# Kernel optimization log

Hardware: AMD Instinct MI355X
Metric: run time of the kernel (lower is better)

The kernel has to match this reference:

```python
import jax, jax.numpy as jnp
import numpy as np

B, S, H = 2, 2048, 2048
FFN = 1024
E = 8
TOP_K = 2


def setup_inputs() -> dict:
    key = jax.random.key(0)
    ks = jax.random.split(key, 5)
    scale = 0.02
    hidden_states = jax.random.normal(ks[0], (B, S, H), dtype=jnp.float32)
    Wg = jax.random.normal(ks[1], (E, H), dtype=jnp.float32) * scale   # gate: Linear(H, E) weight
    W1 = jax.random.normal(ks[2], (E, FFN, H), dtype=jnp.float32) * scale  # stacked w1 per expert
    W3 = jax.random.normal(ks[3], (E, FFN, H), dtype=jnp.float32) * scale  # stacked w3 per expert
    W2 = jax.random.normal(ks[4], (E, H, FFN), dtype=jnp.float32) * scale  # stacked w2 per expert
    bias = jnp.zeros((E,), dtype=jnp.float32)  # e_score_correction_bias buffer
    return {"hidden_states": hidden_states, "Wg": Wg, "W1": W1, "W2": W2, "W3": W3, "bias": bias}


def reference(hidden_states, Wg, W1, W2, W3, bias):
    bsz, seq_len, hidden_dim = hidden_states.shape
    x = hidden_states.reshape(-1, hidden_dim)                 # [T, H]
    router_logits = x @ Wg.T                                  # [T, E]
    routing_weights = jax.nn.sigmoid(router_logits.astype(jnp.float32))
    scores = routing_weights + bias                           # bias only affects selection
    _, top_k_index = jax.lax.top_k(scores, TOP_K)             # [T, K]
    top_k_weights = jnp.take_along_axis(routing_weights, top_k_index, axis=1)
    top_k_weights = top_k_weights / top_k_weights.sum(axis=-1, keepdims=True)
    top_k_weights = top_k_weights.astype(x.dtype)
    # per-token per-expert combine weight (0 for non-selected experts)
    one_hot = jax.nn.one_hot(top_k_index, Wg.shape[0], dtype=x.dtype)  # [T, K, E]
    expert_w = jnp.einsum('tk,tke->te', top_k_weights, one_hot)        # [T, E]
    # SwiGLU expert MLPs applied via stacked (grouped) GEMMs
    h1 = jnp.einsum('th,efh->tef', x, W1)                     # [T, E, FFN]
    h3 = jnp.einsum('th,efh->tef', x, W3)
    g = jax.nn.silu(h1) * h3 * expert_w[:, :, None]           # scale before down-proj
    out = jnp.einsum('tef,ehf->th', g, W2)                    # weighted combine
    return out.reshape(bsz, seq_len, hidden_dim)
```

## Files before the change

### kernel.cpp

```cpp
#include <hip/hip_runtime.h>
#include <hip/hip_bf16.h>


#define T_TOK 4096
#define H_DIM 2048
#define FFN_D 1024
#define NE    8

typedef __attribute__((ext_vector_type(8))) short          bf16x8;
typedef __attribute__((ext_vector_type(4))) float          f32x4;
typedef __attribute__((ext_vector_type(4))) unsigned short us4;

#define N4_PER_W ((size_t)NE * FFN_D * H_DIM / 4)
#define RB_ROUTER 1024u
#define CB_CONV   8192u

__device__ __forceinline__ unsigned short f2bf(float f) {
  unsigned u = __builtin_bit_cast(unsigned, f);
  u += 0x7fffu + ((u >> 16) & 1u);
  return (unsigned short)(u >> 16);
}
__device__ __forceinline__ float bf2f(unsigned short u) {
  return __builtin_bit_cast(float, ((unsigned)u) << 16);
}
__device__ __forceinline__ us4 f4bf(float4 v) {
  union { us4 o; unsigned u[2]; } r;
  asm("v_cvt_pk_bf16_f32 %0, %1, %2" : "=v"(r.u[0]) : "v"(v.x), "v"(v.y));
  asm("v_cvt_pk_bf16_f32 %0, %1, %2" : "=v"(r.u[1]) : "v"(v.z), "v"(v.w));
  return r.o;
}
__device__ __forceinline__ void async16(const void* g, void* l) {
  __builtin_amdgcn_global_load_lds((const __attribute__((address_space(1))) void*)g,
                                   (__attribute__((address_space(3))) void*)l, 16, 0, 0);
}

__global__ void router_conv_kernel(const float* __restrict__ x,
                                   const float* __restrict__ Wg,
                                   const float* __restrict__ bias,
                                   unsigned* __restrict__ epair,
                                   float* __restrict__ wpair,
                                   unsigned short* __restrict__ Xb,
                                   const float* __restrict__ W1, unsigned short* __restrict__ W1b,
                                   const float* __restrict__ W3, unsigned short* __restrict__ W3b) {
  if (blockIdx.x >= RB_ROUTER) {
    size_t b0 = (size_t)(blockIdx.x - RB_ROUTER) * 1024;
#pragma unroll
    for (int k = 0; k < 4; k++) {
      size_t i = b0 + k * 256 + threadIdx.x;
      const float* s; unsigned short* d;
      if (i < N4_PER_W) { s = W1; d = W1b; } else { s = W3; d = W3b; i -= N4_PER_W; }
      float4 v = ((const float4*)s)[i];
      ((us4*)d)[i] = f4bf(v);
    }
    return;
  }
  const int wv   = threadIdx.x >> 6;
  const int lane = threadIdx.x & 63;
  const int t    = blockIdx.x * 4 + wv;

  const float4* xr = (const float4*)(x + (size_t)t * H_DIM);
  us4*          xb = (us4*)(Xb + (size_t)t * H_DIM);

  float acc[NE];
#pragma unroll
  for (int e = 0; e < NE; e++) acc[e] = 0.f;

#pragma unroll
  for (int j = 0; j < 8; j++) {
    int i4 = j * 64 + lane;
    float4 v = xr[i4];
    xb[i4] = f4bf(v);
#pragma unroll
    for (int e = 0; e < NE; e++) {
      float4 w = ((const float4*)(Wg + e * H_DIM))[i4];
      acc[e] += v.x * w.x + v.y * w.y + v.z * w.z + v.w * w.w;
    }
  }
#pragma unroll
  for (int e = 0; e < NE; e++) {
#pragma unroll
    for (int m = 32; m >= 1; m >>= 1) acc[e] += __shfl_xor(acc[e], m, 64);
  }

  if (lane == 0) {
    float sig[NE], sc[NE];
#pragma unroll
    for (int e = 0; e < NE; e++) {
      sig[e] = 1.f / (1.f + expf(-acc[e]));
      sc[e]  = sig[e] + bias[e];
    }
    int i1 = 0; float v1 = sc[0];
#pragma unroll
    for (int e = 1; e < NE; e++) if (sc[e] > v1) { v1 = sc[e]; i1 = e; }
    int i2 = -1; float v2 = -1e30f;
#pragma unroll
    for (int e = 0; e < NE; e++) if (e != i1 && sc[e] > v2) { v2 = sc[e]; i2 = e; }
    float w1 = sig[i1], w2 = sig[i2];
    float s = w1 + w2;
    epair[t] = (unsigned)i1 | ((unsigned)i2 << 8);
    wpair[2 * t]     = w1 / s;
    wpair[2 * t + 1] = w2 / s;
  }
}

__global__ void compact_kernel(const unsigned* __restrict__ epair,
                               const float* __restrict__ wpair,
                               int* __restrict__ cnt,
                               int* __restrict__ base,
                               int* __restrict__ rows,
                               float* __restrict__ wts,
                               int* __restrict__ t2s) {
  const int e    = threadIdx.x >> 6;
  const int lane = threadIdx.x & 63;
  const unsigned long long ltmask = ((unsigned long long)1 << lane) - 1;
  __shared__ int cnts[NE];

  int count = 0;
  for (int c = 0; c < T_TOK; c += 64) {
    int t = c + lane;
    unsigned ep = epair[t];
    bool m1 = ((ep & 255u) == (unsigned)e);
    bool m2 = (((ep >> 8) & 255u) == (unsigned)e);
    unsigned long long b1 = __ballot(m1);
    if (m1) {
      int p = count + __popcll(b1 & ltmask);
      rows[e * T_TOK + p] = t;
      wts [e * T_TOK + p] = wpair[2 * t];
      t2s[2 * t] = (e << 12) | p;
    }
    count += __popcll(b1);
    unsigned long long b2 = __ballot(m2);
    if (m2) {
      int p = count + __popcll(b2 & ltmask);
      rows[e * T_TOK + p] = t;
      wts [e * T_TOK + p] = wpair[2 * t + 1];
      t2s[2 * t + 1] = (e << 12) | p;
    }
    count += __popcll(b2);
  }
  if (lane == 0) { cnts[e] = count; cnt[e] = count; }
  __syncthreads();
  if (threadIdx.x == 0) {
    int s = 0;
    for (int i = 0; i < NE; i++) { base[i] = s; s += cnts[i]; }
    base[NE] = s;
  }
}

__launch_bounds__(256)
__global__ void upproj_fast(const unsigned short* __restrict__ Xb,
                            const unsigned short* __restrict__ W1b,
                            const unsigned short* __restrict__ W3b,
                            const int* __restrict__ cnt,
                            const int* __restrict__ base,
                            const int* __restrict__ rows,
                            const float* __restrict__ wts,
                            unsigned short* __restrict__ G,
                            const float* __restrict__ W2, unsigned short* __restrict__ W2b) {
  if (blockIdx.z == NE) {
    size_t flat = (size_t)blockIdx.y * 16 + blockIdx.x;
    size_t b0 = flat * 8192;
#pragma unroll
    for (int k = 0; k < 32; k++) {
      size_t i = b0 + (size_t)k * 256 + threadIdx.x;
      float4 v = ((const float4*)W2)[i];
      ((us4*)W2b)[i] = f4bf(v);
    }
    return;
  }
  const int e  = blockIdx.z;
  const int m0 = blockIdx.y * 128;
  const int n0 = blockIdx.x * 64;
  const int ce = cnt[e];
  if (m0 >= ce) return;

  __shared__ __align__(16) unsigned short As [3][128 * 32];
  __shared__ __align__(16) unsigned short B1s[3][64 * 32];
  __shared__ __align__(16) unsigned short B3s[3][64 * 32];
  __shared__ int   t_ids[128];
  __shared__ float w_lds[128];

  const int tid = threadIdx.x;
  if (tid < 128) {
    int i = m0 + tid;
    if (i < ce) { t_ids[tid] = rows[e * T_TOK + i]; w_lds[tid] = wts[e * T_TOK + i]; }
    else        { t_ids[tid] = 0;                   w_lds[tid] = 0.f; }
  }
  __syncthreads();

  const int lane = tid & 63;
  const int wv   = tid >> 6;

  const int sA   = (lane >> 3) & 3;
  const int gcol = ((lane & 3) ^ sA) * 8;
  const int rxor = ((lane & 15) >> 1) & 3;
  const int qx   = ((lane >> 4) ^ rxor) * 8;

  const unsigned short* gA[2];
#pragma unroll
  for (int c = 0; c < 2; c++) {
    int r = wv * 32 + c * 16 + (lane >> 2);
    gA[c] = Xb + (size_t)t_ids[r] * H_DIM + gcol;
  }
  const size_t wrow = (size_t)(n0 + wv * 16 + (lane >> 2));
  const unsigned short* gB1 = W1b + (size_t)e * FFN_D * H_DIM + wrow * H_DIM + gcol;
  const unsigned short* gB3 = W3b + (size_t)e * FFN_D * H_DIM + wrow * H_DIM + gcol;
  const int dA0 = (wv * 32 + 0)  * 32;
  const int dA1 = (wv * 32 + 16) * 32;
  const int dB  = (wv * 16) * 32;

  const int wm = (wv & 1) * 64;
  const int wn = (wv >> 1) * 32;
  const int lr = lane & 15;

  f32x4 acc1[4][2], acc3[4][2];
#pragma unroll
  for (int mi = 0; mi < 4; mi++)
#pragma unroll
    for (int ni = 0; ni < 2; ni++) { acc1[mi][ni] = (f32x4)0.f; acc3[mi][ni] = (f32x4)0.f; }

#define STAGE_UP(KT, BUF)                          \
  do {                                             \
    async16(gA[0] + (KT), &As [BUF][dA0]);         \
    async16(gA[1] + (KT), &As [BUF][dA1]);         \
    async16(gB1  + (KT), &B1s[BUF][dB]);           \
    async16(gB3  + (KT), &B3s[BUF][dB]);           \
  } while (0)

  STAGE_UP(0, 0);
  STAGE_UP(32, 1);
  asm volatile("s_waitcnt vmcnt(4)" ::: "memory");
  __builtin_amdgcn_s_barrier();

  for (int k = 0; k < H_DIM / 32; ++k) {
    const int kt2 = (k + 2) * 32;
    const int cb  = k % 3;
    if (kt2 < H_DIM) STAGE_UP(kt2, (k + 2) % 3);
    __builtin_amdgcn_sched_barrier(0);

    bf16x8 a[4], b1[2], b3[2];
#pragma unroll
    for (int mi = 0; mi < 4; mi++)
      a[mi] = *(const bf16x8*)&As[cb][(wm + mi * 16 + lr) * 32 + qx];
#pragma unroll
    for (int ni = 0; ni < 2; ni++) {
      b1[ni] = *(const bf16x8*)&B1s[cb][(wn + ni * 16 + lr) * 32 + qx];
      b3[ni] = *(const bf16x8*)&B3s[cb][(wn + ni * 16 + lr) * 32 + qx];
    }
#pragma unroll
    for (int mi = 0; mi < 4; mi++)
#pragma unroll
      for (int ni = 0; ni < 2; ni++) {
        acc1[mi][ni] = __builtin_amdgcn_mfma_f32_16x16x32_bf16(a[mi], b1[ni], acc1[mi][ni], 0, 0, 0);
        acc3[mi][ni] = __builtin_amdgcn_mfma_f32_16x16x32_bf16(a[mi], b3[ni], acc3[mi][ni], 0, 0, 0);
      }

    if (kt2 < H_DIM) asm volatile("s_waitcnt vmcnt(4)" ::: "memory");
    else             asm volatile("s_waitcnt vmcnt(0)" ::: "memory");
    __builtin_amdgcn_sched_barrier(0);
    __builtin_amdgcn_s_barrier();
    __builtin_amdgcn_sched_barrier(0);
  }
#undef STAGE_UP

  const int be = base[e];
#pragma unroll
  for (int mi = 0; mi < 4; mi++)
#pragma unroll
    for (int ni = 0; ni < 2; ni++)
#pragma unroll
      for (int r = 0; r < 4; r++) {
        int row = wm + mi * 16 + (lane >> 4) * 4 + r;
        int col = wn + ni * 16 + lr;
        int i = m0 + row;
        if (i < ce) {
          float h1 = acc1[mi][ni][r];
          float h3 = acc3[mi][ni][r];
          float g  = h1 / (1.f + expf(-h1)) * h3 * w_lds[row];
          G[(size_t)(be + i) * FFN_D + n0 + col] = f2bf(g);
        }
      }
}

__launch_bounds__(256)
__global__ void downproj_fast(const unsigned short* __restrict__ G,
                              const unsigned short* __restrict__ W2b,
                              const int* __restrict__ cnt,
                              const int* __restrict__ base,
                              unsigned short* __restrict__ Gd) {
  const int e  = blockIdx.z;
  const int m0 = blockIdx.y * 128;
  const int n0 = blockIdx.x * 128;
  const int ce = cnt[e];
  if (m0 >= ce) return;
  const int be = base[e];

  __shared__ __align__(16) unsigned short As[3][128 * 32];
  __shared__ __align__(16) unsigned short Bs[3][128 * 32];

  const int tid  = threadIdx.x;
  const int lane = tid & 63;
  const int wv   = tid >> 6;

  const int sA   = (lane >> 3) & 3;
  const int gcol = ((lane & 3) ^ sA) * 8;
  const int rxor = ((lane & 15) >> 1) & 3;
  const int qx   = ((lane >> 4) ^ rxor) * 8;

  const unsigned short* gA[2];
  const unsigned short* gB[2];
#pragma unroll
  for (int c = 0; c < 2; c++) {
    int r = m0 + wv * 32 + c * 16 + (lane >> 2);
    if (r >= ce) r = ce - 1;
    gA[c] = G + (size_t)(be + r) * FFN_D + gcol;
    int rb = wv * 32 + c * 16 + (lane >> 2);
    gB[c] = W2b + (size_t)e * H_DIM * FFN_D + (size_t)(n0 + rb) * FFN_D + gcol;
  }
  const int dA0 = (wv * 32 + 0)  * 32;
  const int dA1 = (wv * 32 + 16) * 32;

  const int wm = (wv & 1) * 64;
  const int wn = (wv >> 1) * 64;
  const int lr = lane & 15;

  f32x4 acc[4][4];
#pragma unroll
  for (int mi = 0; mi < 4; mi++)
#pragma unroll
    for (int ni = 0; ni < 4; ni++) acc[mi][ni] = (f32x4)0.f;

#define STAGE_DN(KT, BUF)                          \
  do {                                             \
    async16(gA[0] + (KT), &As[BUF][dA0]);          \
    async16(gA[1] + (KT), &As[BUF][dA1]);          \
    async16(gB[0] + (KT), &Bs[BUF][dA0]);          \
    async16(gB[1] + (KT), &Bs[BUF][dA1]);          \
  } while (0)

  STAGE_DN(0, 0);
  STAGE_DN(32, 1);
  asm volatile("s_waitcnt vmcnt(4)" ::: "memory");
  __builtin_amdgcn_s_barrier();

  for (int k = 0; k < FFN_D / 32; ++k) {
    const int kt2 = (k + 2) * 32;
    const int cb  = k % 3;
    if (kt2 < FFN_D) STAGE_DN(kt2, (k + 2) % 3);
    __builtin_amdgcn_sched_barrier(0);

    bf16x8 a[4], b[4];
#pragma unroll
    for (int mi = 0; mi < 4; mi++)
      a[mi] = *(const bf16x8*)&As[cb][(wm + mi * 16 + lr) * 32 + qx];
#pragma unroll
    for (int ni = 0; ni < 4; ni++)
      b[ni] = *(const bf16x8*)&Bs[cb][(wn + ni * 16 + lr) * 32 + qx];
#pragma unroll
    for (int mi = 0; mi < 4; mi++)
#pragma unroll
      for (int ni = 0; ni < 4; ni++)
        acc[mi][ni] = __builtin_amdgcn_mfma_f32_16x16x32_bf16(a[mi], b[ni], acc[mi][ni], 0, 0, 0);

    if (kt2 < FFN_D) asm volatile("s_waitcnt vmcnt(4)" ::: "memory");
    else             asm volatile("s_waitcnt vmcnt(0)" ::: "memory");
    __builtin_amdgcn_sched_barrier(0);
    __builtin_amdgcn_s_barrier();
    __builtin_amdgcn_sched_barrier(0);
  }
#undef STAGE_DN

#pragma unroll
  for (int mi = 0; mi < 4; mi++)
#pragma unroll
    for (int ni = 0; ni < 4; ni++)
#pragma unroll
      for (int r = 0; r < 4; r++) {
        int row = wm + mi * 16 + (lane >> 4) * 4 + r;
        int col = wn + ni * 16 + lr;
        int i = m0 + row;
        if (i < ce)
          Gd[(size_t)(be + i) * H_DIM + n0 + col] = f2bf(acc[mi][ni][r]);
      }
}

__global__ void combine_kernel(const unsigned short* __restrict__ Gd,
                               const int* __restrict__ base,
                               const int* __restrict__ tok2slot,
                               float* __restrict__ out) {
  const int t = blockIdx.x;
  const int v1 = tok2slot[2 * t], v2 = tok2slot[2 * t + 1];
  const int s1 = base[v1 >> 12] + (v1 & 4095);
  const int s2 = base[v2 >> 12] + (v2 & 4095);
  const us4* r1 = (const us4*)(Gd + (size_t)s1 * H_DIM);
  const us4* r2 = (const us4*)(Gd + (size_t)s2 * H_DIM);
  float4* o = (float4*)(out + (size_t)t * H_DIM);
#pragma unroll
  for (int j = 0; j < 2; j++) {
    int i = j * 256 + threadIdx.x;
    us4 a = r1[i], b = r2[i];
    float4 r;
    r.x = bf2f(a.x) + bf2f(b.x);
    r.y = bf2f(a.y) + bf2f(b.y);
    r.z = bf2f(a.z) + bf2f(b.z);
    r.w = bf2f(a.w) + bf2f(b.w);
    o[i] = r;
  }
}

extern "C" void kernel_launch(void* const* d_in, const int* in_sizes, int n_in,
                              void* d_out, int out_size, void* d_ws, size_t ws_size,
                              hipStream_t stream) {
  (void)in_sizes; (void)n_in; (void)out_size; (void)ws_size;
  const float* x    = (const float*)d_in[0];
  const float* Wg   = (const float*)d_in[1];
  const float* W1   = (const float*)d_in[2];
  const float* W2   = (const float*)d_in[3];
  const float* W3   = (const float*)d_in[4];
  const float* bias = (const float*)d_in[5];
  float* out = (float*)d_out;

  char* ws = (char*)d_ws;
  const size_t OFF_CNT   = 0;
  const size_t OFF_BASE  = 64;
  const size_t OFF_T2S   = 1024;
  const size_t OFF_ROWS  = 65536;
  const size_t OFF_WTS   = OFF_ROWS + 131072;
  const size_t OFF_EPAIR = OFF_WTS + 131072;
  const size_t OFF_WPAIR = OFF_EPAIR + 16384;
  const size_t OFF_XB    = 1048576;
  const size_t OFF_W1B   = OFF_XB + 16777216;
  const size_t OFF_W3B   = OFF_W1B + 33554432;
  const size_t OFF_G     = OFF_W3B + 33554432;
  const size_t OFF_W2B   = OFF_G + 16777216;

  int*   cnt   = (int*)(ws + OFF_CNT);
  int*   base  = (int*)(ws + OFF_BASE);
  int*   t2s   = (int*)(ws + OFF_T2S);
  int*   rows  = (int*)(ws + OFF_ROWS);
  float* wts   = (float*)(ws + OFF_WTS);
  unsigned* epair = (unsigned*)(ws + OFF_EPAIR);
  float* wpair = (float*)(ws + OFF_WPAIR);
  unsigned short* Xb  = (unsigned short*)(ws + OFF_XB);
  unsigned short* W1b = (unsigned short*)(ws + OFF_W1B);
  unsigned short* W3b = (unsigned short*)(ws + OFF_W3B);
  unsigned short* W2b = (unsigned short*)(ws + OFF_W2B);
  unsigned short* Gd  = (unsigned short*)(ws + OFF_W1B);
  unsigned short* G   = (unsigned short*)(ws + OFF_G);

  router_conv_kernel<<<RB_ROUTER + CB_CONV, 256, 0, stream>>>(
      x, Wg, bias, epair, wpair, Xb, W1, W1b, W3, W3b);

  compact_kernel<<<1, 512, 0, stream>>>(epair, wpair, cnt, base, rows, wts, t2s);

  dim3 g2(FFN_D / 64, T_TOK / 128, NE + 1);
  upproj_fast<<<g2, 256, 0, stream>>>(Xb, W1b, W3b, cnt, base, rows, wts, G, W2, W2b);

  dim3 g3(H_DIM / 128, T_TOK / 128, NE);
  downproj_fast<<<g3, 256, 0, stream>>>(G, W2b, cnt, base, Gd);

  combine_kernel<<<T_TOK, 256, 0, stream>>>(Gd, base, t2s, out);
}
```

Baseline: 453.3 us.

## Restructure expert GEMMs into 8-wave, 64-deep two-phase pipelined tiles and move W2 conversion

```diff
diff --git a/kernel.cpp b/kernel.cpp
--- a/kernel.cpp
+++ b/kernel.cpp
@@ -14,6 +14,7 @@
 #define N4_PER_W ((size_t)NE * FFN_D * H_DIM / 4)
 #define RB_ROUTER 1024u
 #define CB_CONV   8192u
+#define CB_W2     4096u
 
 __device__ __forceinline__ unsigned short f2bf(float f) {
   unsigned u = __builtin_bit_cast(unsigned, f);
@@ -41,7 +42,18 @@
                                    float* __restrict__ wpair,
                                    unsigned short* __restrict__ Xb,
                                    const float* __restrict__ W1, unsigned short* __restrict__ W1b,
-                                   const float* __restrict__ W3, unsigned short* __restrict__ W3b) {
+                                   const float* __restrict__ W3, unsigned short* __restrict__ W3b,
+                                   const float* __restrict__ W2, unsigned short* __restrict__ W2b) {
+  if (blockIdx.x >= RB_ROUTER + CB_CONV) {
+    size_t b0 = (size_t)(blockIdx.x - RB_ROUTER - CB_CONV) * 1024;
+#pragma unroll
+    for (int k = 0; k < 4; k++) {
+      size_t i = b0 + k * 256 + threadIdx.x;
+      float4 v = ((const float4*)W2)[i];
+      ((us4*)W2b)[i] = f4bf(v);
+    }
+    return;
+  }
   if (blockIdx.x >= RB_ROUTER) {
     size_t b0 = (size_t)(blockIdx.x - RB_ROUTER) * 1024;
 #pragma unroll
@@ -147,71 +159,56 @@
   }
 }
 
-__launch_bounds__(256)
-__global__ void upproj_fast(const unsigned short* __restrict__ Xb,
-                            const unsigned short* __restrict__ W1b,
-                            const unsigned short* __restrict__ W3b,
-                            const int* __restrict__ cnt,
-                            const int* __restrict__ base,
-                            const int* __restrict__ rows,
-                            const float* __restrict__ wts,
-                            unsigned short* __restrict__ G,
-                            const float* __restrict__ W2, unsigned short* __restrict__ W2b) {
-  if (blockIdx.z == NE) {
-    size_t flat = (size_t)blockIdx.y * 16 + blockIdx.x;
-    size_t b0 = flat * 8192;
-#pragma unroll
-    for (int k = 0; k < 32; k++) {
-      size_t i = b0 + (size_t)k * 256 + threadIdx.x;
-      float4 v = ((const float4*)W2)[i];
-      ((us4*)W2b)[i] = f4bf(v);
-    }
-    return;
-  }
+__launch_bounds__(512)
+__global__ void upproj_8ph(const unsigned short* __restrict__ Xb,
+                           const unsigned short* __restrict__ W1b,
+                           const unsigned short* __restrict__ W3b,
+                           const int* __restrict__ cnt,
+                           const int* __restrict__ base,
+                           const int* __restrict__ rows,
+                           const float* __restrict__ wts,
+                           unsigned short* __restrict__ G) {
   const int e  = blockIdx.z;
-  const int m0 = blockIdx.y * 128;
+  const int m0 = blockIdx.y * 256;
   const int n0 = blockIdx.x * 64;
   const int ce = cnt[e];
   if (m0 >= ce) return;
 
-  __shared__ __align__(16) unsigned short As [3][128 * 32];
-  __shared__ __align__(16) unsigned short B1s[3][64 * 32];
-  __shared__ __align__(16) unsigned short B3s[3][64 * 32];
-  __shared__ int   t_ids[128];
-  __shared__ float w_lds[128];
+  __shared__ __align__(16) unsigned short As [3][256 * 64];
+  __shared__ __align__(16) unsigned short B1s[3][64 * 64];
+  __shared__ __align__(16) unsigned short B3s[3][64 * 64];
+  __shared__ int   t_ids[256];
+  __shared__ float w_lds[256];
 
   const int tid = threadIdx.x;
-  if (tid < 128) {
+  if (tid < 256) {
     int i = m0 + tid;
     if (i < ce) { t_ids[tid] = rows[e * T_TOK + i]; w_lds[tid] = wts[e * T_TOK + i]; }
     else        { t_ids[tid] = 0;                   w_lds[tid] = 0.f; }
   }
   __syncthreads();
 
-  const int lane = tid & 63;
-  const int wv   = tid >> 6;
-
-  const int sA   = (lane >> 3) & 3;
-  const int gcol = ((lane & 3) ^ sA) * 8;
-  const int rxor = ((lane & 15) >> 1) & 3;
-  const int qx   = ((lane >> 4) ^ rxor) * 8;
-
-  const unsigned short* gA[2];
-#pragma unroll
-  for (int c = 0; c < 2; c++) {
-    int r = wv * 32 + c * 16 + (lane >> 2);
-    gA[c] = Xb + (size_t)t_ids[r] * H_DIM + gcol;
-  }
-  const size_t wrow = (size_t)(n0 + wv * 16 + (lane >> 2));
-  const unsigned short* gB1 = W1b + (size_t)e * FFN_D * H_DIM + wrow * H_DIM + gcol;
-  const unsigned short* gB3 = W3b + (size_t)e * FFN_D * H_DIM + wrow * H_DIM + gcol;
-  const int dA0 = (wv * 32 + 0)  * 32;
-  const int dA1 = (wv * 32 + 16) * 32;
-  const int dB  = (wv * 16) * 32;
-
-  const int wm = (wv & 1) * 64;
-  const int wn = (wv >> 1) * 32;
-  const int lr = lane & 15;
+  const int lane  = tid & 63;
+  const int wv    = tid >> 6;
+  const int srow8 = lane >> 3;
+  const int scol  = ((lane & 7) ^ srow8) * 8;
+
+  const unsigned short* apA[4];
+#pragma unroll
+  for (int j = 0; j < 4; j++) {
+    int r = j * 64 + wv * 8 + srow8;
+    apA[j] = Xb + (size_t)t_ids[r] * H_DIM + scol;
+  }
+  const size_t ebase = (size_t)e * FFN_D * H_DIM;
+  const int rbw = wv * 8 + srow8;
+  const unsigned short* apB1 = W1b + ebase + (size_t)(n0 + rbw) * H_DIM + scol;
+  const unsigned short* apB3 = W3b + ebase + (size_t)(n0 + rbw) * H_DIM + scol;
+
+  const int wvM = wv >> 1;
+  const int wvN = wv & 1;
+  const int fr  = lane & 15;
+  const int hi  = lane >> 4;
+  const int rx  = fr & 7;
 
   f32x4 acc1[4][2], acc3[4][2];
 #pragma unroll
@@ -219,34 +216,43 @@
 #pragma unroll
     for (int ni = 0; ni < 2; ni++) { acc1[mi][ni] = (f32x4)0.f; acc3[mi][ni] = (f32x4)0.f; }
 
-#define STAGE_UP(KT, BUF)                          \
-  do {                                             \
-    async16(gA[0] + (KT), &As [BUF][dA0]);         \
-    async16(gA[1] + (KT), &As [BUF][dA1]);         \
-    async16(gB1  + (KT), &B1s[BUF][dB]);           \
-    async16(gB3  + (KT), &B3s[BUF][dB]);           \
-  } while (0)
-
-  STAGE_UP(0, 0);
-  STAGE_UP(32, 1);
-  asm volatile("s_waitcnt vmcnt(4)" ::: "memory");
+#define UPS_A3(T, B) { int kk = (T) * 64;                      \
+    async16(apA[0] + kk, &As[B][(  0 + wv * 8) * 64]);         \
+    async16(apA[1] + kk, &As[B][( 64 + wv * 8) * 64]);         \
+    async16(apA[2] + kk, &As[B][(128 + wv * 8) * 64]); }
+#define UPS_AB(T, B) { int kk = (T) * 64;                      \
+    async16(apA[3] + kk, &As[B][(192 + wv * 8) * 64]);         \
+    async16(apB1 + kk,  &B1s[B][(wv * 8) * 64]);               \
+    async16(apB3 + kk,  &B3s[B][(wv * 8) * 64]); }
+
+  UPS_A3(0, 0) UPS_AB(0, 0)
+  UPS_A3(1, 1) UPS_AB(1, 1)
+  asm volatile("s_waitcnt vmcnt(6)" ::: "memory");
   __builtin_amdgcn_s_barrier();
 
-  for (int k = 0; k < H_DIM / 32; ++k) {
-    const int kt2 = (k + 2) * 32;
-    const int cb  = k % 3;
-    if (kt2 < H_DIM) STAGE_UP(kt2, (k + 2) % 3);
-    __builtin_amdgcn_sched_barrier(0);
-
+  for (int t = 0; t < H_DIM / 64; ++t) {
+    const int  cb = t % 3;
+    const int  nb = (t + 2) % 3;
+    const bool pf = (t + 2 < H_DIM / 64);
+
+    if (pf) UPS_A3(t + 2, nb)
     bf16x8 a[4], b1[2], b3[2];
-#pragma unroll
-    for (int mi = 0; mi < 4; mi++)
-      a[mi] = *(const bf16x8*)&As[cb][(wm + mi * 16 + lr) * 32 + qx];
-#pragma unroll
-    for (int ni = 0; ni < 2; ni++) {
-      b1[ni] = *(const bf16x8*)&B1s[cb][(wn + ni * 16 + lr) * 32 + qx];
-      b3[ni] = *(const bf16x8*)&B3s[cb][(wn + ni * 16 + lr) * 32 + qx];
-    }
+    {
+      const int c = ((0 + hi) ^ rx) * 8;
+#pragma unroll
+      for (int mi = 0; mi < 4; mi++)
+        a[mi] = *(const bf16x8*)&As[cb][(wvM * 64 + mi * 16 + fr) * 64 + c];
+#pragma unroll
+      for (int ni = 0; ni < 2; ni++) {
+        b1[ni] = *(const bf16x8*)&B1s[cb][(wvN * 32 + ni * 16 + fr) * 64 + c];
+        b3[ni] = *(const bf16x8*)&B3s[cb][(wvN * 32 + ni * 16 + fr) * 64 + c];
+      }
+    }
+    __builtin_amdgcn_sched_barrier(0);
+    __builtin_amdgcn_s_barrier();
+    asm volatile("s_waitcnt lgkmcnt(0)" ::: "memory");
+    __builtin_amdgcn_sched_barrier(0);
+    __builtin_amdgcn_s_setprio(1);
 #pragma unroll
     for (int mi = 0; mi < 4; mi++)
 #pragma unroll
@@ -254,14 +260,42 @@
         acc1[mi][ni] = __builtin_amdgcn_mfma_f32_16x16x32_bf16(a[mi], b1[ni], acc1[mi][ni], 0, 0, 0);
         acc3[mi][ni] = __builtin_amdgcn_mfma_f32_16x16x32_bf16(a[mi], b3[ni], acc3[mi][ni], 0, 0, 0);
       }
-
-    if (kt2 < H_DIM) asm volatile("s_waitcnt vmcnt(4)" ::: "memory");
-    else             asm volatile("s_waitcnt vmcnt(0)" ::: "memory");
-    __builtin_amdgcn_sched_barrier(0);
-    __builtin_amdgcn_s_barrier();
-    __builtin_amdgcn_sched_barrier(0);
-  }
-#undef STAGE_UP
+    __builtin_amdgcn_s_setprio(0);
+    __builtin_amdgcn_sched_barrier(0);
+    __builtin_amdgcn_s_barrier();
+
+    if (pf) UPS_AB(t + 2, nb)
+    {
+      const int c = ((4 + hi) ^ rx) * 8;
+#pragma unroll
+      for (int mi = 0; mi < 4; mi++)
+        a[mi] = *(const bf16x8*)&As[cb][(wvM * 64 + mi * 16 + fr) * 64 + c];
+#pragma unroll
+      for (int ni = 0; ni < 2; ni++) {
+        b1[ni] = *(const bf16x8*)&B1s[cb][(wvN * 32 + ni * 16 + fr) * 64 + c];
+        b3[ni] = *(const bf16x8*)&B3s[cb][(wvN * 32 + ni * 16 + fr) * 64 + c];
+      }
+    }
+    __builtin_amdgcn_sched_barrier(0);
+    if (pf) asm volatile("s_waitcnt vmcnt(6)" ::: "memory");
+    else    asm volatile("s_waitcnt vmcnt(0)" ::: "memory");
+    __builtin_amdgcn_s_barrier();
+    asm volatile("s_waitcnt lgkmcnt(0)" ::: "memory");
+    __builtin_amdgcn_sched_barrier(0);
+    __builtin_amdgcn_s_setprio(1);
+#pragma unroll
+    for (int mi = 0; mi < 4; mi++)
+#pragma unroll
+      for (int ni = 0; ni < 2; ni++) {
+        acc1[mi][ni] = __builtin_amdgcn_mfma_f32_16x16x32_bf16(a[mi], b1[ni], acc1[mi][ni], 0, 0, 0);
+        acc3[mi][ni] = __builtin_amdgcn_mfma_f32_16x16x32_bf16(a[mi], b3[ni], acc3[mi][ni], 0, 0, 0);
+      }
+    __builtin_amdgcn_s_setprio(0);
+    __builtin_amdgcn_sched_barrier(0);
+    __builtin_amdgcn_s_barrier();
+  }
+#undef UPS_A3
+#undef UPS_AB
 
   const int be = base[e];
 #pragma unroll
@@ -270,8 +304,8 @@
     for (int ni = 0; ni < 2; ni++)
 #pragma unroll
       for (int r = 0; r < 4; r++) {
-        int row = wm + mi * 16 + (lane >> 4) * 4 + r;
-        int col = wn + ni * 16 + lr;
+        int row = wvM * 64 + mi * 16 + hi * 4 + r;
+        int col = wvN * 32 + ni * 16 + fr;
         int i = m0 + row;
         if (i < ce) {
           float h1 = acc1[mi][ni][r];
@@ -282,47 +316,46 @@
       }
 }
 
-__launch_bounds__(256)
-__global__ void downproj_fast(const unsigned short* __restrict__ G,
-                              const unsigned short* __restrict__ W2b,
-                              const int* __restrict__ cnt,
-                              const int* __restrict__ base,
-                              unsigned short* __restrict__ Gd) {
+__launch_bounds__(512)
+__global__ void downproj_8ph(const unsigned short* __restrict__ G,
+                             const unsigned short* __restrict__ W2b,
+                             const int* __restrict__ cnt,
+                             const int* __restrict__ base,
+                             unsigned short* __restrict__ Gd) {
   const int e  = blockIdx.z;
-  const int m0 = blockIdx.y * 128;
+  const int m0 = blockIdx.y * 256;
   const int n0 = blockIdx.x * 128;
   const int ce = cnt[e];
   if (m0 >= ce) return;
   const int be = base[e];
 
-  __shared__ __align__(16) unsigned short As[3][128 * 32];
-  __shared__ __align__(16) unsigned short Bs[3][128 * 32];
-
-  const int tid  = threadIdx.x;
-  const int lane = tid & 63;
-  const int wv   = tid >> 6;
-
-  const int sA   = (lane >> 3) & 3;
-  const int gcol = ((lane & 3) ^ sA) * 8;
-  const int rxor = ((lane & 15) >> 1) & 3;
-  const int qx   = ((lane >> 4) ^ rxor) * 8;
-
-  const unsigned short* gA[2];
-  const unsigned short* gB[2];
-#pragma unroll
-  for (int c = 0; c < 2; c++) {
-    int r = m0 + wv * 32 + c * 16 + (lane >> 2);
-    if (r >= ce) r = ce - 1;
-    gA[c] = G + (size_t)(be + r) * FFN_D + gcol;
-    int rb = wv * 32 + c * 16 + (lane >> 2);
-    gB[c] = W2b + (size_t)e * H_DIM * FFN_D + (size_t)(n0 + rb) * FFN_D + gcol;
-  }
-  const int dA0 = (wv * 32 + 0)  * 32;
-  const int dA1 = (wv * 32 + 16) * 32;
-
-  const int wm = (wv & 1) * 64;
-  const int wn = (wv >> 1) * 64;
-  const int lr = lane & 15;
+  __shared__ __align__(16) unsigned short As[3][256 * 64];
+  __shared__ __align__(16) unsigned short Bs[3][128 * 64];
+
+  const int tid   = threadIdx.x;
+  const int lane  = tid & 63;
+  const int wv    = tid >> 6;
+  const int srow8 = lane >> 3;
+  const int scol  = ((lane & 7) ^ srow8) * 8;
+
+  const unsigned short* apA[4];
+#pragma unroll
+  for (int j = 0; j < 4; j++) {
+    int rr = m0 + j * 64 + wv * 8 + srow8;
+    if (rr >= ce) rr = ce - 1;
+    apA[j] = G + (size_t)(be + rr) * FFN_D + scol;
+  }
+  const unsigned short* apB[2];
+#pragma unroll
+  for (int jb = 0; jb < 2; jb++)
+    apB[jb] = W2b + (size_t)e * H_DIM * FFN_D
+                  + (size_t)(n0 + jb * 64 + wv * 8 + srow8) * FFN_D + scol;
+
+  const int wvM = wv >> 1;
+  const int wvN = wv & 1;
+  const int fr  = lane & 15;
+  const int hi  = lane >> 4;
+  const int rx  = fr & 7;
 
   f32x4 acc[4][4];
 #pragma unroll
@@ -330,45 +363,78 @@
 #pragma unroll
     for (int ni = 0; ni < 4; ni++) acc[mi][ni] = (f32x4)0.f;
 
-#define STAGE_DN(KT, BUF)                          \
-  do {                                             \
-    async16(gA[0] + (KT), &As[BUF][dA0]);          \
-    async16(gA[1] + (KT), &As[BUF][dA1]);          \
-    async16(gB[0] + (KT), &Bs[BUF][dA0]);          \
-    async16(gB[1] + (KT), &Bs[BUF][dA1]);          \
-  } while (0)
-
-  STAGE_DN(0, 0);
-  STAGE_DN(32, 1);
-  asm volatile("s_waitcnt vmcnt(4)" ::: "memory");
+#define DNS_A3(T, B) { int kk = (T) * 64;                      \
+    async16(apA[0] + kk, &As[B][(  0 + wv * 8) * 64]);         \
+    async16(apA[1] + kk, &As[B][( 64 + wv * 8) * 64]);         \
+    async16(apA[2] + kk, &As[B][(128 + wv * 8) * 64]); }
+#define DNS_AB(T, B) { int kk = (T) * 64;                      \
+    async16(apA[3] + kk, &As[B][(192 + wv * 8) * 64]);         \
+    async16(apB[0] + kk, &Bs[B][(  0 + wv * 8) * 64]);         \
+    async16(apB[1] + kk, &Bs[B][( 64 + wv * 8) * 64]); }
+
+  DNS_A3(0, 0) DNS_AB(0, 0)
+  DNS_A3(1, 1) DNS_AB(1, 1)
+  asm volatile("s_waitcnt vmcnt(6)" ::: "memory");
   __builtin_amdgcn_s_barrier();
 
-  for (int k = 0; k < FFN_D / 32; ++k) {
-    const int kt2 = (k + 2) * 32;
-    const int cb  = k % 3;
-    if (kt2 < FFN_D) STAGE_DN(kt2, (k + 2) % 3);
-    __builtin_amdgcn_sched_barrier(0);
-
+  for (int t = 0; t < FFN_D / 64; ++t) {
+    const int  cb = t % 3;
+    const int  nb = (t + 2) % 3;
+    const bool pf = (t + 2 < FFN_D / 64);
+
+    if (pf) DNS_A3(t + 2, nb)
     bf16x8 a[4], b[4];
-#pragma unroll
-    for (int mi = 0; mi < 4; mi++)
-      a[mi] = *(const bf16x8*)&As[cb][(wm + mi * 16 + lr) * 32 + qx];
-#pragma unroll
-    for (int ni = 0; ni < 4; ni++)
-      b[ni] = *(const bf16x8*)&Bs[cb][(wn + ni * 16 + lr) * 32 + qx];
+    {
+      const int c = ((0 + hi) ^ rx) * 8;
+#pragma unroll
+      for (int mi = 0; mi < 4; mi++)
+        a[mi] = *(const bf16x8*)&As[cb][(wvM * 64 + mi * 16 + fr) * 64 + c];
+#pragma unroll
+      for (int ni = 0; ni < 4; ni++)
+        b[ni] = *(const bf16x8*)&Bs[cb][(wvN * 64 + ni * 16 + fr) * 64 + c];
+    }
+    __builtin_amdgcn_sched_barrier(0);
+    __builtin_amdgcn_s_barrier();
+    asm volatile("s_waitcnt lgkmcnt(0)" ::: "memory");
+    __builtin_amdgcn_sched_barrier(0);
+    __builtin_amdgcn_s_setprio(1);
 #pragma unroll
     for (int mi = 0; mi < 4; mi++)
 #pragma unroll
       for (int ni = 0; ni < 4; ni++)
         acc[mi][ni] = __builtin_amdgcn_mfma_f32_16x16x32_bf16(a[mi], b[ni], acc[mi][ni], 0, 0, 0);
-
-    if (kt2 < FFN_D) asm volatile("s_waitcnt vmcnt(4)" ::: "memory");
-    else             asm volatile("s_waitcnt vmcnt(0)" ::: "memory");
-    __builtin_amdgcn_sched_barrier(0);
-    __builtin_amdgcn_s_barrier();
-    __builtin_amdgcn_sched_barrier(0);
-  }
-#undef STAGE_DN
+    __builtin_amdgcn_s_setprio(0);
+    __builtin_amdgcn_sched_barrier(0);
+    __builtin_amdgcn_s_barrier();
+
+    if (pf) DNS_AB(t + 2, nb)
+    {
+      const int c = ((4 + hi) ^ rx) * 8;
+#pragma unroll
+      for (int mi = 0; mi < 4; mi++)
+        a[mi] = *(const bf16x8*)&As[cb][(wvM * 64 + mi * 16 + fr) * 64 + c];
+#pragma unroll
+      for (int ni = 0; ni < 4; ni++)
+        b[ni] = *(const bf16x8*)&Bs[cb][(wvN * 64 + ni * 16 + fr) * 64 + c];
+    }
+    __builtin_amdgcn_sched_barrier(0);
+    if (pf) asm volatile("s_waitcnt vmcnt(6)" ::: "memory");
+    else    asm volatile("s_waitcnt vmcnt(0)" ::: "memory");
+    __builtin_amdgcn_s_barrier();
+    asm volatile("s_waitcnt lgkmcnt(0)" ::: "memory");
+    __builtin_amdgcn_sched_barrier(0);
+    __builtin_amdgcn_s_setprio(1);
+#pragma unroll
+    for (int mi = 0; mi < 4; mi++)
+#pragma unroll
+      for (int ni = 0; ni < 4; ni++)
+        acc[mi][ni] = __builtin_amdgcn_mfma_f32_16x16x32_bf16(a[mi], b[ni], acc[mi][ni], 0, 0, 0);
+    __builtin_amdgcn_s_setprio(0);
+    __builtin_amdgcn_sched_barrier(0);
+    __builtin_amdgcn_s_barrier();
+  }
+#undef DNS_A3
+#undef DNS_AB
 
 #pragma unroll
   for (int mi = 0; mi < 4; mi++)
@@ -376,8 +442,8 @@
     for (int ni = 0; ni < 4; ni++)
 #pragma unroll
       for (int r = 0; r < 4; r++) {
-        int row = wm + mi * 16 + (lane >> 4) * 4 + r;
-        int col = wn + ni * 16 + lr;
+        int row = wvM * 64 + mi * 16 + hi * 4 + r;
+        int col = wvN * 64 + ni * 16 + fr;
         int i = m0 + row;
         if (i < ce)
           Gd[(size_t)(be + i) * H_DIM + n0 + col] = f2bf(acc[mi][ni][r]);
@@ -448,16 +514,16 @@
   unsigned short* Gd  = (unsigned short*)(ws + OFF_W1B);
   unsigned short* G   = (unsigned short*)(ws + OFF_G);
 
-  router_conv_kernel<<<RB_ROUTER + CB_CONV, 256, 0, stream>>>(
-      x, Wg, bias, epair, wpair, Xb, W1, W1b, W3, W3b);
+  router_conv_kernel<<<RB_ROUTER + CB_CONV + CB_W2, 256, 0, stream>>>(
+      x, Wg, bias, epair, wpair, Xb, W1, W1b, W3, W3b, W2, W2b);
 
   compact_kernel<<<1, 512, 0, stream>>>(epair, wpair, cnt, base, rows, wts, t2s);
 
-  dim3 g2(FFN_D / 64, T_TOK / 128, NE + 1);
-  upproj_fast<<<g2, 256, 0, stream>>>(Xb, W1b, W3b, cnt, base, rows, wts, G, W2, W2b);
-
-  dim3 g3(H_DIM / 128, T_TOK / 128, NE);
-  downproj_fast<<<g3, 256, 0, stream>>>(G, W2b, cnt, base, Gd);
+  dim3 g2(FFN_D / 64, T_TOK / 256, NE);
+  upproj_8ph<<<g2, 512, 0, stream>>>(Xb, W1b, W3b, cnt, base, rows, wts, G);
+
+  dim3 g3(H_DIM / 128, T_TOK / 256, NE);
+  downproj_8ph<<<g3, 512, 0, stream>>>(G, W2b, cnt, base, Gd);
 
   combine_kernel<<<T_TOK, 256, 0, stream>>>(Gd, base, t2s, out);
 }
```

Result: slower. 581.9 us (+28.4%).
